# Kernel tuning notes

Hardware: AMD Instinct MI355X
Metric: run time of the kernel (lower is better)

## Reference

```python
import jax, jax.numpy as jnp
import numpy as np

T = 2048      # num_tokens = batch*seq
H = 2048      # hidden_size
E = 64        # num_experts
K = 8         # num_experts_per_tok (top_k)
I = 768       # moe_intermediate_size


def setup_inputs() -> dict:
    key = jax.random.key(0)
    k0, k1, k2, k3, k4 = jax.random.split(key, 5)
    scale = 0.02
    return {
        "hidden_states": jax.random.normal(k0, (T, H), jnp.float32),
        "w_router": jax.random.normal(k1, (E, H), jnp.float32) * scale,   # gate Linear [E, H]
        "w_gate": jax.random.normal(k2, (E, I, H), jnp.float32) * scale,  # per-expert gate_proj
        "w_up": jax.random.normal(k3, (E, I, H), jnp.float32) * scale,    # per-expert up_proj
        "w_down": jax.random.normal(k4, (E, H, I), jnp.float32) * scale,  # per-expert down_proj
    }


def reference(hidden_states, w_router, w_gate, w_up, w_down):
    x = hidden_states                                  # [T, H]
    num_tokens = x.shape[0]
    # --- router ---
    router_logits = x @ w_router.T                     # [T, E]
    probs = jax.nn.softmax(router_logits.astype(jnp.float32), axis=-1)
    top_w, top_i = jax.lax.top_k(probs, K)             # [T, K]
    top_w = top_w / jnp.sum(top_w, axis=-1, keepdims=True)  # norm_topk_prob
    top_w = top_w.astype(x.dtype)
    # dense combine weights [T, E], K nonzeros per row
    combine = jnp.zeros((num_tokens, E), x.dtype).at[
        jnp.arange(num_tokens)[:, None], top_i
    ].set(top_w)
    # --- experts: SwiGLU MLP per expert, weighted combine ---
    def body(acc, params):
        wg, wu, wd, w_e = params                       # [I,H], [I,H], [H,I], [T]
        h = jax.nn.silu(x @ wg.T) * (x @ wu.T)         # [T, I]
        return acc + w_e[:, None] * (h @ wd.T), None
    out, _ = jax.lax.scan(body, jnp.zeros_like(x), (w_gate, w_up, w_down, combine.T))
    return out
```

## Files before the change

### kernel.cpp

```cpp
#include <hip/hip_runtime.h>
#include <hip/hip_fp16.h>

#define T_TOK 2048
#define H_DIM 2048
#define E_NUM 64
#define TOPK  8
#define I_DIM 768

#define BK   32

#define GU_MT 3
#define GU_NT (I_DIM / 64)
#define GU_NWG (GU_MT * GU_NT * E_NUM)
#define DN_MT 3
#define DN_NT (H_DIM / 128)
#define DN_NWG (DN_MT * DN_NT * E_NUM)

using f16x8 = __attribute__((ext_vector_type(8))) _Float16;
using f16x4 = __attribute__((ext_vector_type(4))) _Float16;
using f16x2 = __attribute__((ext_vector_type(2))) _Float16;
using f32x4 = __attribute__((ext_vector_type(4))) float;

__device__ __forceinline__ f16x4 cvt4(float4 v) {
    f16x2 lo = __builtin_bit_cast(f16x2, __builtin_amdgcn_cvt_pkrtz(v.x, v.y));
    f16x2 hi = __builtin_bit_cast(f16x2, __builtin_amdgcn_cvt_pkrtz(v.z, v.w));
    f16x4 o;
    o[0] = lo[0]; o[1] = lo[1]; o[2] = hi[0]; o[3] = hi[1];
    return o;
}
__device__ __forceinline__ f16x8 cvt8(float4 a, float4 b) {
    f16x4 lo = cvt4(a), hi = cvt4(b);
    f16x8 r;
    r[0] = lo[0]; r[1] = lo[1]; r[2] = lo[2]; r[3] = lo[3];
    r[4] = hi[0]; r[5] = hi[1]; r[6] = hi[2]; r[7] = hi[3];
    return r;
}

__device__ __forceinline__ void gload16(const void* g, void* l) {
    __builtin_amdgcn_global_load_lds(
        (const __attribute__((address_space(1))) unsigned int*)g,
        (__attribute__((address_space(3))) unsigned int*)l,
        16, 0, 0);
}

#define BAR()      asm volatile("s_barrier" ::: "memory")
#define VM_WAIT6() asm volatile("s_waitcnt vmcnt(6)" ::: "memory")
#define VM_WAIT0() asm volatile("s_waitcnt vmcnt(0)" ::: "memory")
#define LGKM0()    asm volatile("s_waitcnt lgkmcnt(0)" ::: "memory")

__global__ void convert_x_kernel(const float* __restrict__ x, _Float16* __restrict__ xh, int n) {
    int i = (blockIdx.x * blockDim.x + threadIdx.x) * 4;
    if (i < n) {
        float4 v = *reinterpret_cast<const float4*>(x + i);
        *reinterpret_cast<f16x4*>(xh + i) = cvt4(v);
    }
}

__global__ __launch_bounds__(64) void router_topk_kernel(
        const float* __restrict__ x, const float* __restrict__ wr,
        int* __restrict__ topk_i, float* __restrict__ topk_w) {
    __shared__ float xs[H_DIM];
    int t = blockIdx.x;
    int lane = threadIdx.x;
    const float* xp = x + (size_t)t * H_DIM;
    for (int i = lane * 4; i < H_DIM; i += 64 * 4) {
        *reinterpret_cast<float4*>(xs + i) = *reinterpret_cast<const float4*>(xp + i);
    }
    __syncthreads();
    const float* wp = wr + (size_t)lane * H_DIM;
    float acc = 0.f;
    for (int h = 0; h < H_DIM; h += 4) {
        float4 w = *reinterpret_cast<const float4*>(wp + h);
        acc += xs[h] * w.x + xs[h + 1] * w.y + xs[h + 2] * w.z + xs[h + 3] * w.w;
    }
    float m = acc;
    #pragma unroll
    for (int d = 32; d; d >>= 1) m = fmaxf(m, __shfl_xor(m, d));
    float p = __expf(acc - m);
    float s = p;
    #pragma unroll
    for (int d = 32; d; d >>= 1) s += __shfl_xor(s, d);
    p /= s;
    float selv[TOPK]; int seli[TOPK];
    float cur = p;
    #pragma unroll
    for (int k = 0; k < TOPK; ++k) {
        float v = cur; int idx = lane;
        #pragma unroll
        for (int d = 32; d; d >>= 1) {
            float ov = __shfl_xor(v, d); int oi = __shfl_xor(idx, d);
            if (ov > v || (ov == v && oi < idx)) { v = ov; idx = oi; }
        }
        selv[k] = v; seli[k] = idx;
        if (lane == idx) cur = -1.f;
    }
    float sum = 0.f;
    #pragma unroll
    for (int k = 0; k < TOPK; ++k) sum += selv[k];
    if (lane == 0) {
        #pragma unroll
        for (int k = 0; k < TOPK; ++k) {
            topk_i[t * TOPK + k] = seli[k];
            topk_w[t * TOPK + k] = selv[k] / sum;
        }
    }
}

__global__ void count_kernel(const int* __restrict__ topk_i, int* __restrict__ counts) {
    int i = blockIdx.x * blockDim.x + threadIdx.x;
    if (i < T_TOK * TOPK) atomicAdd(&counts[topk_i[i]], 1);
}

__global__ __launch_bounds__(64) void scan_kernel(const int* __restrict__ counts,
                                                  int* __restrict__ offsets,
                                                  int* __restrict__ cursor) {
    __shared__ int c[E_NUM];
    int e = threadIdx.x;
    c[e] = counts[e];
    __syncthreads();
    int off = 0;
    for (int j = 0; j < e; ++j) off += c[j];
    offsets[e] = off;
    cursor[e] = off;
}

__global__ void scatter_kernel(const int* __restrict__ topk_i, const float* __restrict__ topk_w,
                               int* __restrict__ cursor,
                               int* __restrict__ token_list, float* __restrict__ weight_list) {
    int i = blockIdx.x * blockDim.x + threadIdx.x;
    if (i < T_TOK * TOPK) {
        int e = topk_i[i];
        int pos = atomicAdd(&cursor[e], 1);
        token_list[pos] = i >> 3;
        weight_list[pos] = topk_w[i];
    }
}

__global__ __launch_bounds__(256) void gateup_kernel(
        const _Float16* __restrict__ xh, const float* __restrict__ wg,
        const float* __restrict__ wu, const int* __restrict__ offsets,
        const int* __restrict__ counts, const int* __restrict__ token_list,
        _Float16* __restrict__ hbuf) {
    int orig = blockIdx.x;
    int w = (orig & 7) * (GU_NWG / 8) + (orig >> 3);
    int mt = w % GU_MT;
    int nt = (w / GU_MT) % GU_NT;
    int e  = w / (GU_MT * GU_NT);
    int n_e = counts[e];
    int off_e = offsets[e];
    int n_base = nt * 64;
    const float* wg_e = wg + (size_t)e * I_DIM * H_DIM;
    const float* wu_e = wu + (size_t)e * I_DIM * H_DIM;

    __shared__ __align__(16) _Float16 As[2][128 * 32];
    __shared__ __align__(16) float    Bgs[2][64 * 32];
    __shared__ __align__(16) float    Bus[2][64 * 32];
    __shared__ int toks[128];

    int tid = threadIdx.x;
    int ar = tid >> 2, aslot = tid & 3;
    int acf = aslot ^ (ar & 3);
    int brr = tid >> 3, bslot = tid & 7;
    int bcf = bslot ^ (brr & 7);
    const float* bg0 = wg_e + (size_t)(n_base + brr) * H_DIM + bcf * 4;
    const float* bg1 = wg_e + (size_t)(n_base + 32 + brr) * H_DIM + bcf * 4;
    const float* bu0 = wu_e + (size_t)(n_base + brr) * H_DIM + bcf * 4;
    const float* bu1 = wu_e + (size_t)(n_base + 32 + brr) * H_DIM + bcf * 4;

    int wave = tid >> 6, lane = tid & 63;
    int wm = wave >> 1, wn = wave & 1;
    int aoff[4];
    #pragma unroll
    for (int fm = 0; fm < 4; ++fm) {
        int row = wm * 64 + fm * 16 + (lane & 15);
        aoff[fm] = row * 32 + ((lane >> 4) ^ (lane & 3)) * 8;
    }
    int boff0[2], boff1[2];
    #pragma unroll
    for (int fn = 0; fn < 2; ++fn) {
        int row = wn * 32 + fn * 16 + (lane & 15);
        int c0 = (lane >> 4) * 2;
        boff0[fn] = row * 32 + (c0 ^ (lane & 7)) * 4;
        boff1[fn] = row * 32 + ((c0 + 1) ^ (lane & 7)) * 4;
    }

    for (int m_base = mt * 128; m_base < n_e; m_base += GU_MT * 128) {
        if (tid < 128) toks[tid] = token_list[off_e + min(m_base + tid, n_e - 1)];
        __syncthreads();
        const _Float16* asrc0 = xh + (size_t)toks[ar] * H_DIM + acf * 8;
        const _Float16* asrc1 = xh + (size_t)toks[64 + ar] * H_DIM + acf * 8;

        auto stage = [&](int k0, int b) {
            gload16(asrc0 + k0, &As[b][tid * 8]);
            gload16(asrc1 + k0, &As[b][2048 + tid * 8]);
            gload16(bg0 + k0, &Bgs[b][tid * 4]);
            gload16(bg1 + k0, &Bgs[b][1024 + tid * 4]);
            gload16(bu0 + k0, &Bus[b][tid * 4]);
            gload16(bu1 + k0, &Bus[b][1024 + tid * 4]);
        };

        f32x4 accg[4][2], accu[4][2];
        #pragma unroll
        for (int i = 0; i < 4; ++i)
            #pragma unroll
            for (int j = 0; j < 2; ++j) { accg[i][j] = (f32x4)0.f; accu[i][j] = (f32x4)0.f; }

        auto compute = [&](int b) {
            f16x8 a[4];
            #pragma unroll
            for (int fm = 0; fm < 4; ++fm) a[fm] = *reinterpret_cast<const f16x8*>(&As[b][aoff[fm]]);
            #pragma unroll
            for (int fn = 0; fn < 2; ++fn) {
                float4 g0 = *reinterpret_cast<const float4*>(&Bgs[b][boff0[fn]]);
                float4 g1 = *reinterpret_cast<const float4*>(&Bgs[b][boff1[fn]]);
                float4 u0 = *reinterpret_cast<const float4*>(&Bus[b][boff0[fn]]);
                float4 u1 = *reinterpret_cast<const float4*>(&Bus[b][boff1[fn]]);
                f16x8 bgf = cvt8(g0, g1);
                f16x8 buf = cvt8(u0, u1);
                #pragma unroll
                for (int fm = 0; fm < 4; ++fm) {
                    accg[fm][fn] = __builtin_amdgcn_mfma_f32_16x16x32_f16(a[fm], bgf, accg[fm][fn], 0, 0, 0);
                    accu[fm][fn] = __builtin_amdgcn_mfma_f32_16x16x32_f16(a[fm], buf, accu[fm][fn], 0, 0, 0);
                }
            }
        };

        const int NT = H_DIM / BK;
        stage(0, 0);
        for (int t = 0; t < NT - 1; ++t) {
            stage((t + 1) * BK, (t + 1) & 1);
            VM_WAIT6();
            BAR();
            compute(t & 1);
            LGKM0();
            BAR();
        }
        VM_WAIT0();
        BAR();
        compute((NT - 1) & 1);

        #pragma unroll
        for (int fm = 0; fm < 4; ++fm) {
            #pragma unroll
            for (int reg = 0; reg < 4; ++reg) {
                int row = wm * 64 + fm * 16 + (lane >> 4) * 4 + reg;
                int m = m_base + row;
                if (m < n_e) {
                    #pragma unroll
                    for (int fn = 0; fn < 2; ++fn) {
                        int col = wn * 32 + fn * 16 + (lane & 15);
                        float g = accg[fm][fn][reg];
                        float u = accu[fm][fn][reg];
                        float hv = g * u / (1.f + __expf(-g));
                        hbuf[(size_t)(off_e + m) * I_DIM + n_base + col] = (_Float16)hv;
                    }
                }
            }
        }
        __syncthreads();
    }
}

__global__ __launch_bounds__(256) void down_kernel(
        const _Float16* __restrict__ hbuf, const float* __restrict__ wd,
        const int* __restrict__ offsets, const int* __restrict__ counts,
        const int* __restrict__ token_list, const float* __restrict__ weight_list,
        float* __restrict__ out) {
    int orig = blockIdx.x;
    int w = (orig & 7) * (DN_NWG / 8) + (orig >> 3);
    int mt = w % DN_MT;
    int nt = (w / DN_MT) % DN_NT;
    int e  = w / (DN_MT * DN_NT);
    int n_e = counts[e];
    int off_e = offsets[e];
    int n_base = nt * 128;
    const float* wd_e = wd + (size_t)e * H_DIM * I_DIM;

    __shared__ __align__(16) _Float16 As[2][128 * 32];
    __shared__ __align__(16) float    Bs[2][128 * 32];

    int tid = threadIdx.x;
    int ar = tid >> 2, aslot = tid & 3;
    int acf = aslot ^ (ar & 3);
    int brr = tid >> 3, bslot = tid & 7;
    int bcf = bslot ^ (brr & 7);
    const float* bs0 = wd_e + (size_t)(n_base + brr) * I_DIM + bcf * 4;
    const float* bs1 = bs0 + (size_t)32 * I_DIM;
    const float* bs2 = bs0 + (size_t)64 * I_DIM;
    const float* bs3 = bs0 + (size_t)96 * I_DIM;

    int wave = tid >> 6, lane = tid & 63;
    int wm = wave >> 1, wn = wave & 1;
    int aoff[4];
    #pragma unroll
    for (int fm = 0; fm < 4; ++fm) {
        int row = wm * 64 + fm * 16 + (lane & 15);
        aoff[fm] = row * 32 + ((lane >> 4) ^ (lane & 3)) * 8;
    }
    int boff0[4], boff1[4];
    #pragma unroll
    for (int fn = 0; fn < 4; ++fn) {
        int row = wn * 64 + fn * 16 + (lane & 15);
        int c0 = (lane >> 4) * 2;
        boff0[fn] = row * 32 + (c0 ^ (lane & 7)) * 4;
        boff1[fn] = row * 32 + ((c0 + 1) ^ (lane & 7)) * 4;
    }

    for (int m_base = mt * 128; m_base < n_e; m_base += DN_MT * 128) {
        int am0 = min(m_base + ar, n_e - 1);
        int am1 = min(m_base + 64 + ar, n_e - 1);
        const _Float16* asrc0 = hbuf + (size_t)(off_e + am0) * I_DIM + acf * 8;
        const _Float16* asrc1 = hbuf + (size_t)(off_e + am1) * I_DIM + acf * 8;

        auto stage = [&](int k0, int b) {
            gload16(asrc0 + k0, &As[b][tid * 8]);
            gload16(asrc1 + k0, &As[b][2048 + tid * 8]);
            gload16(bs0 + k0, &Bs[b][tid * 4]);
            gload16(bs1 + k0, &Bs[b][1024 + tid * 4]);
            gload16(bs2 + k0, &Bs[b][2048 + tid * 4]);
            gload16(bs3 + k0, &Bs[b][3072 + tid * 4]);
        };

        f32x4 acc[4][4];
        #pragma unroll
        for (int i = 0; i < 4; ++i)
            #pragma unroll
            for (int j = 0; j < 4; ++j) acc[i][j] = (f32x4)0.f;

        auto compute = [&](int b) {
            f16x8 a[4];
            #pragma unroll
            for (int fm = 0; fm < 4; ++fm) a[fm] = *reinterpret_cast<const f16x8*>(&As[b][aoff[fm]]);
            #pragma unroll
            for (int fn = 0; fn < 4; ++fn) {
                float4 v0 = *reinterpret_cast<const float4*>(&Bs[b][boff0[fn]]);
                float4 v1 = *reinterpret_cast<const float4*>(&Bs[b][boff1[fn]]);
                f16x8 bb = cvt8(v0, v1);
                #pragma unroll
                for (int fm = 0; fm < 4; ++fm)
                    acc[fm][fn] = __builtin_amdgcn_mfma_f32_16x16x32_f16(a[fm], bb, acc[fm][fn], 0, 0, 0);
            }
        };

        const int NT = I_DIM / BK;
        stage(0, 0);
        for (int t = 0; t < NT - 1; ++t) {
            stage((t + 1) * BK, (t + 1) & 1);
            VM_WAIT6();
            BAR();
            compute(t & 1);
            LGKM0();
            BAR();
        }
        VM_WAIT0();
        BAR();
        compute((NT - 1) & 1);

        #pragma unroll
        for (int fm = 0; fm < 4; ++fm) {
            #pragma unroll
            for (int reg = 0; reg < 4; ++reg) {
                int m = m_base + wm * 64 + fm * 16 + (lane >> 4) * 4 + reg;
                if (m < n_e) {
                    int slot = off_e + m;
                    int t = token_list[slot];
                    float wt = weight_list[slot];
                    float* orow = out + (size_t)t * H_DIM + n_base;
                    #pragma unroll
                    for (int fn = 0; fn < 4; ++fn) {
                        int col = wn * 64 + fn * 16 + (lane & 15);
                        atomicAdd(orow + col, wt * acc[fm][fn][reg]);
                    }
                }
            }
        }
        __syncthreads();
    }
}

extern "C" void kernel_launch(void* const* d_in, const int* in_sizes, int n_in,
                              void* d_out, int out_size, void* d_ws, size_t ws_size,
                              hipStream_t stream) {
    const float* x  = (const float*)d_in[0];
    const float* wr = (const float*)d_in[1];
    const float* wg = (const float*)d_in[2];
    const float* wu = (const float*)d_in[3];
    const float* wd = (const float*)d_in[4];
    float* out = (float*)d_out;

    char* p = (char*)d_ws;
    auto carve = [&](size_t bytes) { char* q = p; p += (bytes + 255) & ~255ULL; return q; };
    _Float16* xh     = (_Float16*)carve((size_t)T_TOK * H_DIM * 2);
    _Float16* hbuf   = (_Float16*)carve((size_t)T_TOK * TOPK * I_DIM * 2);
    int*   topk_i    = (int*)  carve(T_TOK * TOPK * 4);
    float* topk_w    = (float*)carve(T_TOK * TOPK * 4);
    int*   tlist     = (int*)  carve(T_TOK * TOPK * 4);
    float* wlist     = (float*)carve(T_TOK * TOPK * 4);
    int*   counts    = (int*)  carve(E_NUM * 4);
    int*   offsets   = (int*)  carve(E_NUM * 4);
    int*   cursor    = (int*)  carve(E_NUM * 4);

    (void)hipMemsetAsync(d_out, 0, (size_t)out_size * 4, stream);
    (void)hipMemsetAsync(counts, 0, E_NUM * 4, stream);

    convert_x_kernel<<<(T_TOK * H_DIM) / (256 * 4), 256, 0, stream>>>(x, xh, T_TOK * H_DIM);
    router_topk_kernel<<<T_TOK, 64, 0, stream>>>(x, wr, topk_i, topk_w);
    count_kernel<<<(T_TOK * TOPK) / 256, 256, 0, stream>>>(topk_i, counts);
    scan_kernel<<<1, 64, 0, stream>>>(counts, offsets, cursor);
    scatter_kernel<<<(T_TOK * TOPK) / 256, 256, 0, stream>>>(topk_i, topk_w, cursor, tlist, wlist);
    gateup_kernel<<<GU_NWG, 256, 0, stream>>>(xh, wg, wu, offsets, counts, tlist, hbuf);
    down_kernel<<<DN_NWG, 256, 0, stream>>>(hbuf, wd, offsets, counts, tlist, wlist, out);
}
```

Measured before the change: 819.0 us.

## Load expert weights directly into registers, bypassing LDS, in both GEMM kernels

Measured after the change: 763.5 us. -6.8%, faster.

```diff
diff --git a/kernel.cpp b/kernel.cpp
--- a/kernel.cpp
+++ b/kernel.cpp
@@ -136,7 +136,7 @@
     }
 }
 
-__global__ __launch_bounds__(256) void gateup_kernel(
+__global__ __launch_bounds__(256, 3) void gateup_kernel(
         const _Float16* __restrict__ xh, const float* __restrict__ wg,
         const float* __restrict__ wu, const int* __restrict__ offsets,
         const int* __restrict__ counts, const int* __restrict__ token_list,
@@ -153,35 +153,23 @@
     const float* wu_e = wu + (size_t)e * I_DIM * H_DIM;
 
     __shared__ __align__(16) _Float16 As[2][128 * 32];
-    __shared__ __align__(16) float    Bgs[2][64 * 32];
-    __shared__ __align__(16) float    Bus[2][64 * 32];
     __shared__ int toks[128];
 
     int tid = threadIdx.x;
     int ar = tid >> 2, aslot = tid & 3;
     int acf = aslot ^ (ar & 3);
-    int brr = tid >> 3, bslot = tid & 7;
-    int bcf = bslot ^ (brr & 7);
-    const float* bg0 = wg_e + (size_t)(n_base + brr) * H_DIM + bcf * 4;
-    const float* bg1 = wg_e + (size_t)(n_base + 32 + brr) * H_DIM + bcf * 4;
-    const float* bu0 = wu_e + (size_t)(n_base + brr) * H_DIM + bcf * 4;
-    const float* bu1 = wu_e + (size_t)(n_base + 32 + brr) * H_DIM + bcf * 4;
-
-    int wave = tid >> 6, lane = tid & 63;
-    int wm = wave >> 1, wn = wave & 1;
-    int aoff[4];
-    #pragma unroll
-    for (int fm = 0; fm < 4; ++fm) {
-        int row = wm * 64 + fm * 16 + (lane & 15);
+    int wn = tid >> 6, lane = tid & 63;
+    int lrow = lane & 15;
+    int kgrp = lane >> 4;
+
+    const float* gp = wg_e + (size_t)(n_base + wn * 16 + lrow) * H_DIM + kgrp * 8;
+    const float* up = wu_e + (size_t)(n_base + wn * 16 + lrow) * H_DIM + kgrp * 8;
+
+    int aoff[8];
+    #pragma unroll
+    for (int fm = 0; fm < 8; ++fm) {
+        int row = fm * 16 + lrow;
         aoff[fm] = row * 32 + ((lane >> 4) ^ (lane & 3)) * 8;
-    }
-    int boff0[2], boff1[2];
-    #pragma unroll
-    for (int fn = 0; fn < 2; ++fn) {
-        int row = wn * 32 + fn * 16 + (lane & 15);
-        int c0 = (lane >> 4) * 2;
-        boff0[fn] = row * 32 + (c0 ^ (lane & 7)) * 4;
-        boff1[fn] = row * 32 + ((c0 + 1) ^ (lane & 7)) * 4;
     }
 
     for (int m_base = mt * 128; m_base < n_e; m_base += GU_MT * 128) {
@@ -190,78 +178,92 @@
         const _Float16* asrc0 = xh + (size_t)toks[ar] * H_DIM + acf * 8;
         const _Float16* asrc1 = xh + (size_t)toks[64 + ar] * H_DIM + acf * 8;
 
-        auto stage = [&](int k0, int b) {
+        f32x4 accg[8], accu[8];
+        #pragma unroll
+        for (int i = 0; i < 8; ++i) { accg[i] = (f32x4)0.f; accu[i] = (f32x4)0.f; }
+
+        float4 gA0, gA1, uA0, uA1;
+        float4 gB0, gB1, uB0, uB1;
+
+        auto stageA = [&](int k0, int b) {
             gload16(asrc0 + k0, &As[b][tid * 8]);
             gload16(asrc1 + k0, &As[b][2048 + tid * 8]);
-            gload16(bg0 + k0, &Bgs[b][tid * 4]);
-            gload16(bg1 + k0, &Bgs[b][1024 + tid * 4]);
-            gload16(bu0 + k0, &Bus[b][tid * 4]);
-            gload16(bu1 + k0, &Bus[b][1024 + tid * 4]);
         };
-
-        f32x4 accg[4][2], accu[4][2];
-        #pragma unroll
-        for (int i = 0; i < 4; ++i)
+        auto compute = [&](int b, float4 g0, float4 g1, float4 u0, float4 u1) {
+            f16x8 bg = cvt8(g0, g1);
+            f16x8 bu = cvt8(u0, u1);
             #pragma unroll
-            for (int j = 0; j < 2; ++j) { accg[i][j] = (f32x4)0.f; accu[i][j] = (f32x4)0.f; }
-
-        auto compute = [&](int b) {
-            f16x8 a[4];
+            for (int fm = 0; fm < 8; ++fm) {
+                f16x8 a = *reinterpret_cast<const f16x8*>(&As[b][aoff[fm]]);
+                accg[fm] = __builtin_amdgcn_mfma_f32_16x16x32_f16(a, bg, accg[fm], 0, 0, 0);
+                accu[fm] = __builtin_amdgcn_mfma_f32_16x16x32_f16(a, bu, accu[fm], 0, 0, 0);
+            }
+        };
+
+        const int NT = H_DIM / BK;
+        stageA(0, 0);
+        gA0 = *reinterpret_cast<const float4*>(gp);
+        gA1 = *reinterpret_cast<const float4*>(gp + 4);
+        uA0 = *reinterpret_cast<const float4*>(up);
+        uA1 = *reinterpret_cast<const float4*>(up + 4);
+        for (int t = 0; t + 2 < NT; t += 2) {
+            int k1 = (t + 1) * BK, k2 = (t + 2) * BK;
+            stageA(k1, 1);
+            gB0 = *reinterpret_cast<const float4*>(gp + k1);
+            gB1 = *reinterpret_cast<const float4*>(gp + k1 + 4);
+            uB0 = *reinterpret_cast<const float4*>(up + k1);
+            uB1 = *reinterpret_cast<const float4*>(up + k1 + 4);
+            VM_WAIT6();
+            BAR();
+            compute(0, gA0, gA1, uA0, uA1);
+            LGKM0();
+            BAR();
+            stageA(k2, 0);
+            gA0 = *reinterpret_cast<const float4*>(gp + k2);
+            gA1 = *reinterpret_cast<const float4*>(gp + k2 + 4);
+            uA0 = *reinterpret_cast<const float4*>(up + k2);
+            uA1 = *reinterpret_cast<const float4*>(up + k2 + 4);
+            VM_WAIT6();
+            BAR();
+            compute(1, gB0, gB1, uB0, uB1);
+            LGKM0();
+            BAR();
+        }
+        {
+            int k1 = (NT - 1) * BK;
+            stageA(k1, 1);
+            gB0 = *reinterpret_cast<const float4*>(gp + k1);
+            gB1 = *reinterpret_cast<const float4*>(gp + k1 + 4);
+            uB0 = *reinterpret_cast<const float4*>(up + k1);
+            uB1 = *reinterpret_cast<const float4*>(up + k1 + 4);
+            VM_WAIT6();
+            BAR();
+            compute(0, gA0, gA1, uA0, uA1);
+            LGKM0();
+            BAR();
+            VM_WAIT0();
+            BAR();
+            compute(1, gB0, gB1, uB0, uB1);
+        }
+
+        #pragma unroll
+        for (int fm = 0; fm < 8; ++fm) {
             #pragma unroll
-            for (int fm = 0; fm < 4; ++fm) a[fm] = *reinterpret_cast<const f16x8*>(&As[b][aoff[fm]]);
-            #pragma unroll
-            for (int fn = 0; fn < 2; ++fn) {
-                float4 g0 = *reinterpret_cast<const float4*>(&Bgs[b][boff0[fn]]);
-                float4 g1 = *reinterpret_cast<const float4*>(&Bgs[b][boff1[fn]]);
-                float4 u0 = *reinterpret_cast<const float4*>(&Bus[b][boff0[fn]]);
-                float4 u1 = *reinterpret_cast<const float4*>(&Bus[b][boff1[fn]]);
-                f16x8 bgf = cvt8(g0, g1);
-                f16x8 buf = cvt8(u0, u1);
-                #pragma unroll
-                for (int fm = 0; fm < 4; ++fm) {
-                    accg[fm][fn] = __builtin_amdgcn_mfma_f32_16x16x32_f16(a[fm], bgf, accg[fm][fn], 0, 0, 0);
-                    accu[fm][fn] = __builtin_amdgcn_mfma_f32_16x16x32_f16(a[fm], buf, accu[fm][fn], 0, 0, 0);
+            for (int reg = 0; reg < 4; ++reg) {
+                int m = m_base + fm * 16 + kgrp * 4 + reg;
+                if (m < n_e) {
+                    float g = accg[fm][reg];
+                    float u = accu[fm][reg];
+                    float hv = g * u / (1.f + __expf(-g));
+                    hbuf[(size_t)(off_e + m) * I_DIM + n_base + wn * 16 + lrow] = (_Float16)hv;
                 }
             }
-        };
-
-        const int NT = H_DIM / BK;
-        stage(0, 0);
-        for (int t = 0; t < NT - 1; ++t) {
-            stage((t + 1) * BK, (t + 1) & 1);
-            VM_WAIT6();
-            BAR();
-            compute(t & 1);
-            LGKM0();
-            BAR();
-        }
-        VM_WAIT0();
-        BAR();
-        compute((NT - 1) & 1);
-
-        #pragma unroll
-        for (int fm = 0; fm < 4; ++fm) {
-            #pragma unroll
-            for (int reg = 0; reg < 4; ++reg) {
-                int row = wm * 64 + fm * 16 + (lane >> 4) * 4 + reg;
-                int m = m_base + row;
-                if (m < n_e) {
-                    #pragma unroll
-                    for (int fn = 0; fn < 2; ++fn) {
-                        int col = wn * 32 + fn * 16 + (lane & 15);
-                        float g = accg[fm][fn][reg];
-                        float u = accu[fm][fn][reg];
-                        float hv = g * u / (1.f + __expf(-g));
-                        hbuf[(size_t)(off_e + m) * I_DIM + n_base + col] = (_Float16)hv;
-                    }
-                }
-            }
         }
         __syncthreads();
     }
 }
 
-__global__ __launch_bounds__(256) void down_kernel(
+__global__ __launch_bounds__(256, 3) void down_kernel(
         const _Float16* __restrict__ hbuf, const float* __restrict__ wd,
         const int* __restrict__ offsets, const int* __restrict__ counts,
         const int* __restrict__ token_list, const float* __restrict__ weight_list,
@@ -277,33 +279,23 @@
     const float* wd_e = wd + (size_t)e * H_DIM * I_DIM;
 
     __shared__ __align__(16) _Float16 As[2][128 * 32];
-    __shared__ __align__(16) float    Bs[2][128 * 32];
-
     int tid = threadIdx.x;
     int ar = tid >> 2, aslot = tid & 3;
     int acf = aslot ^ (ar & 3);
-    int brr = tid >> 3, bslot = tid & 7;
-    int bcf = bslot ^ (brr & 7);
-    const float* bs0 = wd_e + (size_t)(n_base + brr) * I_DIM + bcf * 4;
-    const float* bs1 = bs0 + (size_t)32 * I_DIM;
-    const float* bs2 = bs0 + (size_t)64 * I_DIM;
-    const float* bs3 = bs0 + (size_t)96 * I_DIM;
-
-    int wave = tid >> 6, lane = tid & 63;
-    int wm = wave >> 1, wn = wave & 1;
-    int aoff[4];
-    #pragma unroll
-    for (int fm = 0; fm < 4; ++fm) {
-        int row = wm * 64 + fm * 16 + (lane & 15);
+    int wn = tid >> 6, lane = tid & 63;
+    int lrow = lane & 15;
+    int kgrp = lane >> 4;
+    int col0 = n_base + wn * 32 + lrow;
+    int col1 = col0 + 16;
+
+    const float* bp0 = wd_e + (size_t)col0 * I_DIM + kgrp * 8;
+    const float* bp1 = wd_e + (size_t)col1 * I_DIM + kgrp * 8;
+
+    int aoff[8];
+    #pragma unroll
+    for (int fm = 0; fm < 8; ++fm) {
+        int row = fm * 16 + lrow;
         aoff[fm] = row * 32 + ((lane >> 4) ^ (lane & 3)) * 8;
-    }
-    int boff0[4], boff1[4];
-    #pragma unroll
-    for (int fn = 0; fn < 4; ++fn) {
-        int row = wn * 64 + fn * 16 + (lane & 15);
-        int c0 = (lane >> 4) * 2;
-        boff0[fn] = row * 32 + (c0 ^ (lane & 7)) * 4;
-        boff1[fn] = row * 32 + ((c0 + 1) ^ (lane & 7)) * 4;
     }
 
     for (int m_base = mt * 128; m_base < n_e; m_base += DN_MT * 128) {
@@ -312,65 +304,86 @@
         const _Float16* asrc0 = hbuf + (size_t)(off_e + am0) * I_DIM + acf * 8;
         const _Float16* asrc1 = hbuf + (size_t)(off_e + am1) * I_DIM + acf * 8;
 
-        auto stage = [&](int k0, int b) {
+        f32x4 acc0[8], acc1[8];
+        #pragma unroll
+        for (int i = 0; i < 8; ++i) { acc0[i] = (f32x4)0.f; acc1[i] = (f32x4)0.f; }
+
+        float4 aA0, aA1, bA0, bA1;
+        float4 aB0, aB1, bB0, bB1;
+
+        auto stageA = [&](int k0, int b) {
             gload16(asrc0 + k0, &As[b][tid * 8]);
             gload16(asrc1 + k0, &As[b][2048 + tid * 8]);
-            gload16(bs0 + k0, &Bs[b][tid * 4]);
-            gload16(bs1 + k0, &Bs[b][1024 + tid * 4]);
-            gload16(bs2 + k0, &Bs[b][2048 + tid * 4]);
-            gload16(bs3 + k0, &Bs[b][3072 + tid * 4]);
         };
-
-        f32x4 acc[4][4];
-        #pragma unroll
-        for (int i = 0; i < 4; ++i)
+        auto compute = [&](int b, float4 v00, float4 v01, float4 v10, float4 v11) {
+            f16x8 bb0 = cvt8(v00, v01);
+            f16x8 bb1 = cvt8(v10, v11);
             #pragma unroll
-            for (int j = 0; j < 4; ++j) acc[i][j] = (f32x4)0.f;
-
-        auto compute = [&](int b) {
-            f16x8 a[4];
-            #pragma unroll
-            for (int fm = 0; fm < 4; ++fm) a[fm] = *reinterpret_cast<const f16x8*>(&As[b][aoff[fm]]);
-            #pragma unroll
-            for (int fn = 0; fn < 4; ++fn) {
-                float4 v0 = *reinterpret_cast<const float4*>(&Bs[b][boff0[fn]]);
-                float4 v1 = *reinterpret_cast<const float4*>(&Bs[b][boff1[fn]]);
-                f16x8 bb = cvt8(v0, v1);
-                #pragma unroll
-                for (int fm = 0; fm < 4; ++fm)
-                    acc[fm][fn] = __builtin_amdgcn_mfma_f32_16x16x32_f16(a[fm], bb, acc[fm][fn], 0, 0, 0);
+            for (int fm = 0; fm < 8; ++fm) {
+                f16x8 a = *reinterpret_cast<const f16x8*>(&As[b][aoff[fm]]);
+                acc0[fm] = __builtin_amdgcn_mfma_f32_16x16x32_f16(a, bb0, acc0[fm], 0, 0, 0);
+                acc1[fm] = __builtin_amdgcn_mfma_f32_16x16x32_f16(a, bb1, acc1[fm], 0, 0, 0);
             }
         };
 
         const int NT = I_DIM / BK;
-        stage(0, 0);
-        for (int t = 0; t < NT - 1; ++t) {
-            stage((t + 1) * BK, (t + 1) & 1);
-            VM_WAIT6();
-            BAR();
-            compute(t & 1);
-            LGKM0();
-            BAR();
-        }
-        VM_WAIT0();
-        BAR();
-        compute((NT - 1) & 1);
-
-        #pragma unroll
-        for (int fm = 0; fm < 4; ++fm) {
+        stageA(0, 0);
+        aA0 = *reinterpret_cast<const float4*>(bp0);
+        aA1 = *reinterpret_cast<const float4*>(bp0 + 4);
+        bA0 = *reinterpret_cast<const float4*>(bp1);
+        bA1 = *reinterpret_cast<const float4*>(bp1 + 4);
+        for (int t = 0; t + 2 < NT; t += 2) {
+            int k1 = (t + 1) * BK, k2 = (t + 2) * BK;
+            stageA(k1, 1);
+            aB0 = *reinterpret_cast<const float4*>(bp0 + k1);
+            aB1 = *reinterpret_cast<const float4*>(bp0 + k1 + 4);
+            bB0 = *reinterpret_cast<const float4*>(bp1 + k1);
+            bB1 = *reinterpret_cast<const float4*>(bp1 + k1 + 4);
+            VM_WAIT6();
+            BAR();
+            compute(0, aA0, aA1, bA0, bA1);
+            LGKM0();
+            BAR();
+            stageA(k2, 0);
+            aA0 = *reinterpret_cast<const float4*>(bp0 + k2);
+            aA1 = *reinterpret_cast<const float4*>(bp0 + k2 + 4);
+            bA0 = *reinterpret_cast<const float4*>(bp1 + k2);
+            bA1 = *reinterpret_cast<const float4*>(bp1 + k2 + 4);
+            VM_WAIT6();
+            BAR();
+            compute(1, aB0, aB1, bB0, bB1);
+            LGKM0();
+            BAR();
+        }
+        {
+            int k1 = (NT - 1) * BK;
+            stageA(k1, 1);
+            aB0 = *reinterpret_cast<const float4*>(bp0 + k1);
+            aB1 = *reinterpret_cast<const float4*>(bp0 + k1 + 4);
+            bB0 = *reinterpret_cast<const float4*>(bp1 + k1);
+            bB1 = *reinterpret_cast<const float4*>(bp1 + k1 + 4);
+            VM_WAIT6();
+            BAR();
+            compute(0, aA0, aA1, bA0, bA1);
+            LGKM0();
+            BAR();
+            VM_WAIT0();
+            BAR();
+            compute(1, aB0, aB1, bB0, bB1);
+        }
+
+        #pragma unroll
+        for (int fm = 0; fm < 8; ++fm) {
             #pragma unroll
             for (int reg = 0; reg < 4; ++reg) {
-                int m = m_base + wm * 64 + fm * 16 + (lane >> 4) * 4 + reg;
+                int m = m_base + fm * 16 + kgrp * 4 + reg;
                 if (m < n_e) {
                     int slot = off_e + m;
                     int t = token_list[slot];
                     float wt = weight_list[slot];
-                    float* orow = out + (size_t)t * H_DIM + n_base;
-                    #pragma unroll
-                    for (int fn = 0; fn < 4; ++fn) {
-                        int col = wn * 64 + fn * 16 + (lane & 15);
-                        atomicAdd(orow + col, wt * acc[fm][fn][reg]);
-                    }
+                    float* orow = out + (size_t)t * H_DIM;
+                    atomicAdd(orow + col0, wt * acc0[fm][reg]);
+                    atomicAdd(orow + col1, wt * acc1[fm][reg]);
                 }
             }
         }
```
